# Performance work log

Measured on AMD Instinct MI355X. Metric: run time of the kernel, lower is better.

Reference implementation:

```python
import jax, jax.numpy as jnp
import numpy as np

FEATURE_DIM = 4
LOSS_WEIGHT = 1.0
DELTA_V = 0.5
DELTA_D = 1.5
NUM_INST = 16  # labels 0..15 all present w.h.p. -> torch.unique yields exactly these


def _safe_norm(x, axis):
    # L2 norm with zero-safe gradient (relu clamp downstream kills grad anyway)
    sq = jnp.sum(x * x, axis=axis)
    return jnp.where(sq > 0, jnp.sqrt(jnp.where(sq > 0, sq, 1.0)), 0.0)


def _forward_single(emb, instance, kernel, training_mask):
    # emb: [D, H, W]; instance/kernel/training_mask: [H, W]
    D, K = FEATURE_DIM, NUM_INST
    tm = (training_mask > 0.5).astype(jnp.int32)
    kn = (kernel > 0.5).astype(jnp.int32)
    inst = instance * tm                      # [H, W]
    inst_k = (inst * kn).reshape(-1)          # [N]
    inst = inst.reshape(-1)                   # [N]
    embf = emb.reshape(D, -1).T               # [N, D]

    # per-instance mean over kernel pixels (scatter-mean); label 0 stays zero
    cnt_k = jax.ops.segment_sum(jnp.ones(inst_k.shape, jnp.float32), inst_k, K)
    sum_k = jax.ops.segment_sum(embf, inst_k, K)          # [K, D]
    emb_mean = sum_k / jnp.maximum(cnt_k, 1.0)[:, None]
    emb_mean = emb_mean.at[0].set(0.0)

    # l_agg: per-pixel distance to own-instance mean, segment-mean per label
    dist = _safe_norm(embf - emb_mean[inst], axis=1)       # [N]
    val = jnp.log(jax.nn.relu(dist - DELTA_V) ** 2 + 1.0)
    cnt = jax.ops.segment_sum(jnp.ones(inst.shape, jnp.float32), inst, K)
    agg = jax.ops.segment_sum(val, inst, K) / jnp.maximum(cnt, 1.0)
    l_agg = jnp.mean(agg[1:])

    # l_dis: pairwise means, excluding diagonal and label 0
    diff = emb_mean[:, None, :] - emb_mean[None, :, :]     # [K, K, D]
    pd = _safe_norm(diff, axis=-1)
    pv = jnp.log(jax.nn.relu(2.0 * DELTA_D - pd) ** 2 + 1.0)
    mask = 1.0 - jnp.eye(K, dtype=jnp.float32)
    mask = mask.at[0, :].set(0.0).at[:, 0].set(0.0)
    l_dis = jnp.sum(pv * mask) / ((K - 1) * (K - 2))

    # l_reg: mean log(||mean_i|| + 1) over ALL K columns (incl. zero col 0)
    l_reg = jnp.mean(jnp.log(_safe_norm(emb_mean, axis=1) + 1.0)) * 0.001

    return l_agg + l_dis + l_reg


def reference(emb, instance, kernel, training_mask, bboxes):
    # bboxes is accepted but unused, as in the original forward
    loss_batch = jax.vmap(_forward_single)(emb, instance, kernel, training_mask)
    return jnp.mean(LOSS_WEIGHT * loss_batch)


def setup_inputs() -> dict:
    key = jax.random.key(0)
    k1, k2, k3, k4, k5 = jax.random.split(key, 5)
    B, H, W = 8, 640, 640
    return {
        "emb": jax.random.normal(k1, (B, FEATURE_DIM, H, W), jnp.float32),
        "instance": jax.random.randint(k2, (B, H, W), 0, NUM_INST, jnp.int32),
        "kernel": jax.random.uniform(k3, (B, H, W), dtype=jnp.float32),
        "training_mask": jax.random.uniform(k4, (B, H, W), dtype=jnp.float32),
        "bboxes": jax.random.uniform(k5, (B, 201, 4), dtype=jnp.float32),
    }
```

## Files before the change

### kernel.cpp

```cpp
#include <hip/hip_runtime.h>
#include <math.h>

#define NUM_K 16
#define FD 4
#define DELTA_V 0.5f
#define DELTA_D 1.5f


__global__ __launch_bounds__(256) void pass1_kernel(
    const float* __restrict__ emb, const int* __restrict__ inst,
    const float* __restrict__ kern, const float* __restrict__ tmask,
    float* __restrict__ cntk, float* __restrict__ sumk, int N)
{
    const int b = blockIdx.y;
    __shared__ float s_cnt[NUM_K];
    __shared__ float s_sum[NUM_K][FD];

    for (int i = threadIdx.x; i < NUM_K; i += blockDim.x) {
        s_cnt[i] = 0.f;
        #pragma unroll
        for (int d = 0; d < FD; ++d) s_sum[i][d] = 0.f;
    }
    __syncthreads();

    const size_t base = (size_t)b * N;
    const int4*   iv4 = (const int4*)(inst + base);
    const float4* kv4 = (const float4*)(kern + base);
    const float4* tv4 = (const float4*)(tmask + base);
    const float4* e0v = (const float4*)(emb + ((size_t)b * FD + 0) * N);
    const float4* e1v = (const float4*)(emb + ((size_t)b * FD + 1) * N);
    const float4* e2v = (const float4*)(emb + ((size_t)b * FD + 2) * N);
    const float4* e3v = (const float4*)(emb + ((size_t)b * FD + 3) * N);

    const int ng = N >> 2;
    for (int g = blockIdx.x * blockDim.x + threadIdx.x; g < ng;
         g += gridDim.x * blockDim.x) {
        int4   iv = iv4[g];
        float4 kv = kv4[g];
        float4 tv = tv4[g];
        float4 a0 = e0v[g], a1 = e1v[g], a2 = e2v[g], a3 = e3v[g];

        #define ACC(px)                                                        \
            {                                                                  \
                int lab = (tv.px > 0.5f) ? iv.px : 0;                          \
                if (lab > 0 && kv.px > 0.5f) {                                 \
                    atomicAdd(&s_cnt[lab], 1.f);                               \
                    atomicAdd(&s_sum[lab][0], a0.px);                          \
                    atomicAdd(&s_sum[lab][1], a1.px);                          \
                    atomicAdd(&s_sum[lab][2], a2.px);                          \
                    atomicAdd(&s_sum[lab][3], a3.px);                          \
                }                                                              \
            }
        ACC(x) ACC(y) ACC(z) ACC(w)
        #undef ACC
    }
    __syncthreads();

    for (int i = threadIdx.x; i < NUM_K; i += blockDim.x) {
        if (s_cnt[i] != 0.f) {
            atomicAdd(&cntk[b * NUM_K + i], s_cnt[i]);
            #pragma unroll
            for (int d = 0; d < FD; ++d)
                atomicAdd(&sumk[(b * NUM_K + i) * FD + d], s_sum[i][d]);
        }
    }
}

__global__ __launch_bounds__(256) void pass2_kernel(
    const float* __restrict__ emb, const int* __restrict__ inst,
    const float* __restrict__ tmask,
    const float* __restrict__ cntk, const float* __restrict__ sumk,
    float* __restrict__ vsum, float* __restrict__ vcnt, int N)
{
    const int b = blockIdx.y;
    __shared__ float s_mean[NUM_K][FD];
    __shared__ float s_vs[NUM_K];
    __shared__ float s_vc[NUM_K];

    if (threadIdx.x < NUM_K * FD) {
        int k = threadIdx.x >> 2, d = threadIdx.x & 3;
        float c = cntk[b * NUM_K + k];
        float m = (k == 0) ? 0.f
                           : sumk[(b * NUM_K + k) * FD + d] / fmaxf(c, 1.f);
        s_mean[k][d] = m;
    }
    if (threadIdx.x < NUM_K) { s_vs[threadIdx.x] = 0.f; s_vc[threadIdx.x] = 0.f; }
    __syncthreads();

    const size_t base = (size_t)b * N;
    const int4*   iv4 = (const int4*)(inst + base);
    const float4* tv4 = (const float4*)(tmask + base);
    const float4* e0v = (const float4*)(emb + ((size_t)b * FD + 0) * N);
    const float4* e1v = (const float4*)(emb + ((size_t)b * FD + 1) * N);
    const float4* e2v = (const float4*)(emb + ((size_t)b * FD + 2) * N);
    const float4* e3v = (const float4*)(emb + ((size_t)b * FD + 3) * N);

    const int ng = N >> 2;
    for (int g = blockIdx.x * blockDim.x + threadIdx.x; g < ng;
         g += gridDim.x * blockDim.x) {
        int4   iv = iv4[g];
        float4 tv = tv4[g];
        float4 a0 = e0v[g], a1 = e1v[g], a2 = e2v[g], a3 = e3v[g];

        #define DIST(px)                                                       \
            {                                                                  \
                int lab = (tv.px > 0.5f) ? iv.px : 0;                          \
                if (lab > 0) {                                                 \
                    float dx = a0.px - s_mean[lab][0];                         \
                    float dy = a1.px - s_mean[lab][1];                         \
                    float dz = a2.px - s_mean[lab][2];                         \
                    float dw = a3.px - s_mean[lab][3];                         \
                    float dist = sqrtf(dx*dx + dy*dy + dz*dz + dw*dw);         \
                    float r = fmaxf(dist - DELTA_V, 0.f);                      \
                    float val = logf(r * r + 1.f);                             \
                    atomicAdd(&s_vs[lab], val);                                \
                    atomicAdd(&s_vc[lab], 1.f);                                \
                }                                                              \
            }
        DIST(x) DIST(y) DIST(z) DIST(w)
        #undef DIST
    }
    __syncthreads();

    for (int i = threadIdx.x; i < NUM_K; i += blockDim.x) {
        if (s_vc[i] != 0.f) {
            atomicAdd(&vsum[b * NUM_K + i], s_vs[i]);
            atomicAdd(&vcnt[b * NUM_K + i], s_vc[i]);
        }
    }
}

__global__ __launch_bounds__(128) void finalize_kernel(
    const float* __restrict__ cntk, const float* __restrict__ sumk,
    const float* __restrict__ vsum, const float* __restrict__ vcnt,
    float* __restrict__ out, int B)
{
    __shared__ float s_mean[8][NUM_K][FD];
    __shared__ float s_part[128];

    const int t = threadIdx.x;
    const int b = t >> 4;
    const int k = t & 15;

    float c = cntk[t];
    float m0 = 0.f, m1 = 0.f, m2 = 0.f, m3 = 0.f;
    if (k != 0) {
        float inv = 1.f / fmaxf(c, 1.f);
        m0 = sumk[t * FD + 0] * inv;
        m1 = sumk[t * FD + 1] * inv;
        m2 = sumk[t * FD + 2] * inv;
        m3 = sumk[t * FD + 3] * inv;
    }
    s_mean[b][k][0] = m0; s_mean[b][k][1] = m1;
    s_mean[b][k][2] = m2; s_mean[b][k][3] = m3;
    __syncthreads();

    float partial = 0.f;

    if (k >= 1) {
        float agg = vsum[t] / fmaxf(vcnt[t], 1.f);
        partial += agg / 15.f;
    }

    if (k >= 1) {
        #pragma unroll
        for (int j = 1; j < NUM_K; ++j) {
            if (j == k) continue;
            float dx = m0 - s_mean[b][j][0];
            float dy = m1 - s_mean[b][j][1];
            float dz = m2 - s_mean[b][j][2];
            float dw = m3 - s_mean[b][j][3];
            float sq = dx*dx + dy*dy + dz*dz + dw*dw;
            float pd = sqrtf(sq);
            float r = fmaxf(2.f * DELTA_D - pd, 0.f);
            partial += logf(r * r + 1.f) / 210.f;
        }
    }

    {
        float nrm = sqrtf(m0*m0 + m1*m1 + m2*m2 + m3*m3);
        partial += logf(nrm + 1.f) * (0.001f / 16.f);
    }

    s_part[t] = partial;
    __syncthreads();

    if (t == 0) {
        float s = 0.f;
        for (int i = 0; i < 128; ++i) s += s_part[i];
        out[0] = s / (float)B;
    }
}

extern "C" void kernel_launch(void* const* d_in, const int* in_sizes, int n_in,
                              void* d_out, int out_size, void* d_ws, size_t ws_size,
                              hipStream_t stream) {
    const float* emb   = (const float*)d_in[0];
    const int*   inst  = (const int*)d_in[1];
    const float* kern  = (const float*)d_in[2];
    const float* tmask = (const float*)d_in[3];

    const int B = 8;
    const int N = in_sizes[1] / B;

    float* ws   = (float*)d_ws;
    float* cntk = ws;
    float* sumk = ws + 128;
    float* vsum = ws + 640;
    float* vcnt = ws + 768;
    float* outf = (float*)d_out;

    hipMemsetAsync(d_ws, 0, 896 * sizeof(float), stream);

    dim3 blk(256);
    dim3 grd(128, B);
    pass1_kernel<<<grd, blk, 0, stream>>>(emb, inst, kern, tmask, cntk, sumk, N);
    pass2_kernel<<<grd, blk, 0, stream>>>(emb, inst, tmask, cntk, sumk, vsum, vcnt, N);
    finalize_kernel<<<dim3(1), dim3(128), 0, stream>>>(cntk, sumk, vsum, vcnt, outf, B);
}
```

Measured before the change: 166.8 us.

## Replace shared-memory atomics with per-thread register histograms and wave reductions

Both passes drop their per-pixel LDS atomicAdd histograms, which contend heavily across only 16 labels. Each thread now keeps 15 per-label accumulators in registers, updated branch-free with select-and-FMA over every label. Wave shuffle reductions and a small LDS cross-wave sum produce the block totals. This removes atomic serialization but costs about 15x more ALU work per pixel and many registers, with launch bounds set to keep occupancy at 4 blocks.

```diff
diff --git a/kernel.cpp b/kernel.cpp
--- a/kernel.cpp
+++ b/kernel.cpp
@@ -7,21 +7,19 @@
 #define DELTA_D 1.5f
 
 
-__global__ __launch_bounds__(256) void pass1_kernel(
+__global__ __launch_bounds__(256, 4) void pass1_kernel(
     const float* __restrict__ emb, const int* __restrict__ inst,
     const float* __restrict__ kern, const float* __restrict__ tmask,
     float* __restrict__ cntk, float* __restrict__ sumk, int N)
 {
     const int b = blockIdx.y;
-    __shared__ float s_cnt[NUM_K];
-    __shared__ float s_sum[NUM_K][FD];
-
-    for (int i = threadIdx.x; i < NUM_K; i += blockDim.x) {
-        s_cnt[i] = 0.f;
-        #pragma unroll
-        for (int d = 0; d < FD; ++d) s_sum[i][d] = 0.f;
-    }
-    __syncthreads();
+
+    float acc[15][5];
+    #pragma unroll
+    for (int k = 0; k < 15; ++k) {
+        #pragma unroll
+        for (int v = 0; v < 5; ++v) acc[k][v] = 0.f;
+    }
 
     const size_t base = (size_t)b * N;
     const int4*   iv4 = (const int4*)(inst + base);
@@ -42,50 +40,76 @@
 
         #define ACC(px)                                                        \
             {                                                                  \
-                int lab = (tv.px > 0.5f) ? iv.px : 0;                          \
-                if (lab > 0 && kv.px > 0.5f) {                                 \
-                    atomicAdd(&s_cnt[lab], 1.f);                               \
-                    atomicAdd(&s_sum[lab][0], a0.px);                          \
-                    atomicAdd(&s_sum[lab][1], a1.px);                          \
-                    atomicAdd(&s_sum[lab][2], a2.px);                          \
-                    atomicAdd(&s_sum[lab][3], a3.px);                          \
+                const int   lab = iv.px;                                       \
+                const float am  = (tv.px > 0.5f && kv.px > 0.5f) ? 1.f : 0.f;  \
+                _Pragma("unroll")                                              \
+                for (int k = 1; k < 16; ++k) {                                 \
+                    const float s = (lab == k) ? am : 0.f;                     \
+                    acc[k-1][4] += s;                                          \
+                    acc[k-1][0] = fmaf(s, a0.px, acc[k-1][0]);                 \
+                    acc[k-1][1] = fmaf(s, a1.px, acc[k-1][1]);                 \
+                    acc[k-1][2] = fmaf(s, a2.px, acc[k-1][2]);                 \
+                    acc[k-1][3] = fmaf(s, a3.px, acc[k-1][3]);                 \
                 }                                                              \
             }
         ACC(x) ACC(y) ACC(z) ACC(w)
         #undef ACC
     }
-    __syncthreads();
-
-    for (int i = threadIdx.x; i < NUM_K; i += blockDim.x) {
-        if (s_cnt[i] != 0.f) {
-            atomicAdd(&cntk[b * NUM_K + i], s_cnt[i]);
+
+    #pragma unroll
+    for (int k = 0; k < 15; ++k) {
+        #pragma unroll
+        for (int v = 0; v < 5; ++v) {
+            float x = acc[k][v];
             #pragma unroll
-            for (int d = 0; d < FD; ++d)
-                atomicAdd(&sumk[(b * NUM_K + i) * FD + d], s_sum[i][d]);
-        }
-    }
-}
-
-__global__ __launch_bounds__(256) void pass2_kernel(
+            for (int m = 32; m > 0; m >>= 1) x += __shfl_xor(x, m, 64);
+            acc[k][v] = x;
+        }
+    }
+
+    __shared__ float s_red[4][75];
+    const int lane = threadIdx.x & 63, wid = threadIdx.x >> 6;
+    if (lane == 0) {
+        #pragma unroll
+        for (int k = 0; k < 15; ++k) {
+            #pragma unroll
+            for (int v = 0; v < 5; ++v) s_red[wid][k * 5 + v] = acc[k][v];
+        }
+    }
+    __syncthreads();
+
+    const int t = threadIdx.x;
+    if (t < 75) {
+        float s = s_red[0][t] + s_red[1][t] + s_red[2][t] + s_red[3][t];
+        const int k = t / 5 + 1, v = t % 5;
+        if (s != 0.f) {
+            if (v < 4) atomicAdd(&sumk[(b * NUM_K + k) * FD + v], s);
+            else       atomicAdd(&cntk[b * NUM_K + k], s);
+        }
+    }
+}
+
+__global__ __launch_bounds__(256, 4) void pass2_kernel(
     const float* __restrict__ emb, const int* __restrict__ inst,
     const float* __restrict__ tmask,
     const float* __restrict__ cntk, const float* __restrict__ sumk,
     float* __restrict__ vsum, float* __restrict__ vcnt, int N)
 {
     const int b = blockIdx.y;
-    __shared__ float s_mean[NUM_K][FD];
-    __shared__ float s_vs[NUM_K];
-    __shared__ float s_vc[NUM_K];
+    __shared__ float4 s_mean[NUM_K];
 
     if (threadIdx.x < NUM_K * FD) {
-        int k = threadIdx.x >> 2, d = threadIdx.x & 3;
-        float c = cntk[b * NUM_K + k];
-        float m = (k == 0) ? 0.f
-                           : sumk[(b * NUM_K + k) * FD + d] / fmaxf(c, 1.f);
-        s_mean[k][d] = m;
-    }
-    if (threadIdx.x < NUM_K) { s_vs[threadIdx.x] = 0.f; s_vc[threadIdx.x] = 0.f; }
-    __syncthreads();
+        const int k = threadIdx.x >> 2, d = threadIdx.x & 3;
+        const float c = cntk[b * NUM_K + k];
+        const float m = (k == 0) ? 0.f
+                                 : sumk[(b * NUM_K + k) * FD + d] / fmaxf(c, 1.f);
+        ((float*)&s_mean[k])[d] = m;
+    }
+    __syncthreads();
+
+    float acc[15][2];
+    #pragma unroll
+    for (int k = 0; k < 15; ++k) { acc[k][0] = 0.f; acc[k][1] = 0.f; }
 
     const size_t base = (size_t)b * N;
     const int4*   iv4 = (const int4*)(inst + base);
@@ -104,28 +128,55 @@
 
         #define DIST(px)                                                       \
             {                                                                  \
-                int lab = (tv.px > 0.5f) ? iv.px : 0;                          \
-                if (lab > 0) {                                                 \
-                    float dx = a0.px - s_mean[lab][0];                         \
-                    float dy = a1.px - s_mean[lab][1];                         \
-                    float dz = a2.px - s_mean[lab][2];                         \
-                    float dw = a3.px - s_mean[lab][3];                         \
-                    float dist = sqrtf(dx*dx + dy*dy + dz*dz + dw*dw);         \
-                    float r = fmaxf(dist - DELTA_V, 0.f);                      \
-                    float val = logf(r * r + 1.f);                             \
-                    atomicAdd(&s_vs[lab], val);                                \
-                    atomicAdd(&s_vc[lab], 1.f);                                \
+                const int lab = (tv.px > 0.5f) ? iv.px : 0;                    \
+                float4 mu = s_mean[lab];                                       \
+                float dx = a0.px - mu.x;                                       \
+                float dy = a1.px - mu.y;                                       \
+                float dz = a2.px - mu.z;                                       \
+                float dw = a3.px - mu.w;                                       \
+                float dist = sqrtf(dx*dx + dy*dy + dz*dz + dw*dw);             \
+                float r = fmaxf(dist - DELTA_V, 0.f);                          \
+                float val = logf(fmaf(r, r, 1.f));                             \
+                _Pragma("unroll")                                              \
+                for (int k = 1; k < 16; ++k) {                                 \
+                    const float s = (lab == k) ? 1.f : 0.f;                    \
+                    acc[k-1][0] = fmaf(s, val, acc[k-1][0]);                   \
+                    acc[k-1][1] += s;                                          \
                 }                                                              \
             }
         DIST(x) DIST(y) DIST(z) DIST(w)
         #undef DIST
     }
-    __syncthreads();
-
-    for (int i = threadIdx.x; i < NUM_K; i += blockDim.x) {
-        if (s_vc[i] != 0.f) {
-            atomicAdd(&vsum[b * NUM_K + i], s_vs[i]);
-            atomicAdd(&vcnt[b * NUM_K + i], s_vc[i]);
+
+    #pragma unroll
+    for (int k = 0; k < 15; ++k) {
+        #pragma unroll
+        for (int v = 0; v < 2; ++v) {
+            float x = acc[k][v];
+            #pragma unroll
+            for (int m = 32; m > 0; m >>= 1) x += __shfl_xor(x, m, 64);
+            acc[k][v] = x;
+        }
+    }
+
+    __shared__ float s_red[4][30];
+    const int lane = threadIdx.x & 63, wid = threadIdx.x >> 6;
+    if (lane == 0) {
+        #pragma unroll
+        for (int k = 0; k < 15; ++k) {
+            s_red[wid][k * 2 + 0] = acc[k][0];
+            s_red[wid][k * 2 + 1] = acc[k][1];
+        }
+    }
+    __syncthreads();
+
+    const int t = threadIdx.x;
+    if (t < 30) {
+        float s = s_red[0][t] + s_red[1][t] + s_red[2][t] + s_red[3][t];
+        const int k = (t >> 1) + 1;
+        if (s != 0.f) {
+            if ((t & 1) == 0) atomicAdd(&vsum[b * NUM_K + k], s);
+            else              atomicAdd(&vcnt[b * NUM_K + k], s);
         }
     }
 }
```

New measurement: 183.3 us. +9.9%, slower.

## Privatize shared-memory histograms per lane to cut atomic contention

Applied to the files above, without the earlier changes.

Both scatter passes switch from one shared-memory accumulator per label to 64 lane-private copies per label, laid out with a stride of 65 to avoid bank conflicts. At the end of each block the copies are reduced by a small set of threads before the global atomics. This targets the heavy serialization from many lanes doing shared atomics on only 16 addresses. The grid is also doubled to 256 blocks per batch, and the extra shared-memory zeroing and reduction add per-block overhead.

```diff
diff --git a/kernel.cpp b/kernel.cpp
--- a/kernel.cpp
+++ b/kernel.cpp
@@ -12,16 +12,12 @@
     const float* __restrict__ kern, const float* __restrict__ tmask,
     float* __restrict__ cntk, float* __restrict__ sumk, int N)
 {
-    const int b = blockIdx.y;
-    __shared__ float s_cnt[NUM_K];
-    __shared__ float s_sum[NUM_K][FD];
-
-    for (int i = threadIdx.x; i < NUM_K; i += blockDim.x) {
-        s_cnt[i] = 0.f;
-        #pragma unroll
-        for (int d = 0; d < FD; ++d) s_sum[i][d] = 0.f;
-    }
-    __syncthreads();
+    __shared__ float s_h[75 * 65];
+    for (int i = threadIdx.x; i < 75 * 65; i += 256) s_h[i] = 0.f;
+    __syncthreads();
+
+    const int b    = blockIdx.y;
+    const int copy = threadIdx.x & 63;
 
     const size_t base = (size_t)b * N;
     const int4*   iv4 = (const int4*)(inst + base);
@@ -42,13 +38,14 @@
 
         #define ACC(px)                                                        \
             {                                                                  \
-                int lab = (tv.px > 0.5f) ? iv.px : 0;                          \
-                if (lab > 0 && kv.px > 0.5f) {                                 \
-                    atomicAdd(&s_cnt[lab], 1.f);                               \
-                    atomicAdd(&s_sum[lab][0], a0.px);                          \
-                    atomicAdd(&s_sum[lab][1], a1.px);                          \
-                    atomicAdd(&s_sum[lab][2], a2.px);                          \
-                    atomicAdd(&s_sum[lab][3], a3.px);                          \
+                const int lab = iv.px;                                         \
+                if (lab > 0 && tv.px > 0.5f && kv.px > 0.5f) {                 \
+                    float* p = &s_h[(lab - 1) * 325 + copy];                   \
+                    atomicAdd(p + 0 * 65, a0.px);                              \
+                    atomicAdd(p + 1 * 65, a1.px);                              \
+                    atomicAdd(p + 2 * 65, a2.px);                              \
+                    atomicAdd(p + 3 * 65, a3.px);                              \
+                    atomicAdd(p + 4 * 65, 1.f);                                \
                 }                                                              \
             }
         ACC(x) ACC(y) ACC(z) ACC(w)
@@ -56,12 +53,14 @@
     }
     __syncthreads();
 
-    for (int i = threadIdx.x; i < NUM_K; i += blockDim.x) {
-        if (s_cnt[i] != 0.f) {
-            atomicAdd(&cntk[b * NUM_K + i], s_cnt[i]);
-            #pragma unroll
-            for (int d = 0; d < FD; ++d)
-                atomicAdd(&sumk[(b * NUM_K + i) * FD + d], s_sum[i][d]);
+    const int t = threadIdx.x;
+    if (t < 75) {
+        float s = 0.f;
+        for (int c = 0; c < 64; ++c) s += s_h[t * 65 + c];
+        if (s != 0.f) {
+            const int k = t / 5 + 1, v = t % 5;
+            if (v < 4) atomicAdd(&sumk[(b * NUM_K + k) * FD + v], s);
+            else       atomicAdd(&cntk[b * NUM_K + k], s);
         }
     }
 }
@@ -72,20 +71,22 @@
     const float* __restrict__ cntk, const float* __restrict__ sumk,
     float* __restrict__ vsum, float* __restrict__ vcnt, int N)
 {
+    __shared__ float  s_h[30 * 65];
+    __shared__ float4 s_mean[NUM_K];
+
+    for (int i = threadIdx.x; i < 30 * 65; i += 256) s_h[i] = 0.f;
+
     const int b = blockIdx.y;
-    __shared__ float s_mean[NUM_K][FD];
-    __shared__ float s_vs[NUM_K];
-    __shared__ float s_vc[NUM_K];
-
     if (threadIdx.x < NUM_K * FD) {
-        int k = threadIdx.x >> 2, d = threadIdx.x & 3;
-        float c = cntk[b * NUM_K + k];
-        float m = (k == 0) ? 0.f
-                           : sumk[(b * NUM_K + k) * FD + d] / fmaxf(c, 1.f);
-        s_mean[k][d] = m;
-    }
-    if (threadIdx.x < NUM_K) { s_vs[threadIdx.x] = 0.f; s_vc[threadIdx.x] = 0.f; }
-    __syncthreads();
+        const int k = threadIdx.x >> 2, d = threadIdx.x & 3;
+        const float c = cntk[b * NUM_K + k];
+        const float m = (k == 0) ? 0.f
+                                 : sumk[(b * NUM_K + k) * FD + d] / fmaxf(c, 1.f);
+        ((float*)&s_mean[k])[d] = m;
+    }
+    __syncthreads();
+
+    const int copy = threadIdx.x & 63;
 
     const size_t base = (size_t)b * N;
     const int4*   iv4 = (const int4*)(inst + base);
@@ -104,17 +105,19 @@
 
         #define DIST(px)                                                       \
             {                                                                  \
-                int lab = (tv.px > 0.5f) ? iv.px : 0;                          \
+                const int lab = (tv.px > 0.5f) ? iv.px : 0;                    \
                 if (lab > 0) {                                                 \
-                    float dx = a0.px - s_mean[lab][0];                         \
-                    float dy = a1.px - s_mean[lab][1];                         \
-                    float dz = a2.px - s_mean[lab][2];                         \
-                    float dw = a3.px - s_mean[lab][3];                         \
+                    float4 mu = s_mean[lab];                                   \
+                    float dx = a0.px - mu.x;                                   \
+                    float dy = a1.px - mu.y;                                   \
+                    float dz = a2.px - mu.z;                                   \
+                    float dw = a3.px - mu.w;                                   \
                     float dist = sqrtf(dx*dx + dy*dy + dz*dz + dw*dw);         \
                     float r = fmaxf(dist - DELTA_V, 0.f);                      \
-                    float val = logf(r * r + 1.f);                             \
-                    atomicAdd(&s_vs[lab], val);                                \
-                    atomicAdd(&s_vc[lab], 1.f);                                \
+                    float val = logf(fmaf(r, r, 1.f));                         \
+                    float* p = &s_h[(lab - 1) * 130 + copy];                   \
+                    atomicAdd(p,      val);                                    \
+                    atomicAdd(p + 65, 1.f);                                    \
                 }                                                              \
             }
         DIST(x) DIST(y) DIST(z) DIST(w)
@@ -122,10 +125,14 @@
     }
     __syncthreads();
 
-    for (int i = threadIdx.x; i < NUM_K; i += blockDim.x) {
-        if (s_vc[i] != 0.f) {
-            atomicAdd(&vsum[b * NUM_K + i], s_vs[i]);
-            atomicAdd(&vcnt[b * NUM_K + i], s_vc[i]);
+    const int t = threadIdx.x;
+    if (t < 30) {
+        float s = 0.f;
+        for (int c = 0; c < 64; ++c) s += s_h[t * 65 + c];
+        if (s != 0.f) {
+            const int k = (t >> 1) + 1;
+            if ((t & 1) == 0) atomicAdd(&vsum[b * NUM_K + k], s);
+            else              atomicAdd(&vcnt[b * NUM_K + k], s);
         }
     }
 }
@@ -213,7 +220,7 @@
     hipMemsetAsync(d_ws, 0, 896 * sizeof(float), stream);
 
     dim3 blk(256);
-    dim3 grd(128, B);
+    dim3 grd(256, B);
     pass1_kernel<<<grd, blk, 0, stream>>>(emb, inst, kern, tmask, cntk, sumk, N);
     pass2_kernel<<<grd, blk, 0, stream>>>(emb, inst, tmask, cntk, sumk, vsum, vcnt, N);
     finalize_kernel<<<dim3(1), dim3(128), 0, stream>>>(cntk, sumk, vsum, vcnt, outf, B);
```

Result: faster. 163.5 us (-2.0%).
